# Kernel optimization log

Hardware: AMD Instinct MI355X
Metric: run time of the kernel (lower is better)

## Reference

```python
import jax, jax.numpy as jnp
import numpy as np

N, E, IN = 50000, 800000, 64
HC, FC1, FC2, FC3, OUT = 96, 256, 128, 64, 8
EPS = 1e-5


def setup_inputs() -> dict:
    key = jax.random.key(0)
    ks = jax.random.split(key, 24)
    def lin(k, fi, fo):
        # kaiming_uniform with relu gain: bound = sqrt(6/fi)
        b = np.sqrt(6.0 / fi)
        return jax.random.uniform(k, (fi, fo), jnp.float32, -b, b)
    inp = {
        'x': jax.random.normal(ks[0], (N, IN), jnp.float32),
        'edge_index': jax.random.randint(ks[1], (2, E), 0, N, jnp.int64),
        'w1': lin(ks[2], IN, HC), 'b1': jnp.zeros((HC,), jnp.float32),
        'g1': jax.random.uniform(ks[3], (HC,), jnp.float32, 0.5, 1.5), 'be1': jax.random.normal(ks[4], (HC,), jnp.float32) * 0.1,
        'w2': lin(ks[5], HC, HC), 'b2': jnp.zeros((HC,), jnp.float32),
        'g2': jax.random.uniform(ks[6], (HC,), jnp.float32, 0.5, 1.5), 'be2': jax.random.normal(ks[7], (HC,), jnp.float32) * 0.1,
        'w3': lin(ks[8], HC, HC), 'b3': jnp.zeros((HC,), jnp.float32),
        'g3': jax.random.uniform(ks[9], (HC,), jnp.float32, 0.5, 1.5), 'be3': jax.random.normal(ks[10], (HC,), jnp.float32) * 0.1,
        'lw1': lin(ks[11], HC, FC1), 'lb1': jnp.zeros((FC1,), jnp.float32),
        'lw2': lin(ks[12], FC1, FC2), 'lb2': jnp.zeros((FC2,), jnp.float32),
        'lw3': lin(ks[13], FC2, FC3), 'lb3': jnp.zeros((FC3,), jnp.float32),
        'lw4': lin(ks[14], FC3, OUT), 'lb4': jnp.zeros((OUT,), jnp.float32),
    }
    return inp


def _gcn(x, w, b, src, dst, norm):
    # GCNConv: out[dst] += norm_e * (x @ w)[src]; then + bias
    h = x @ w
    msg = h[src] * norm[:, None]
    return jax.ops.segment_sum(msg, dst, num_segments=N) + b


def _bn_eval(x, g, be):
    # eval-mode BatchNorm1d with running_mean=0, running_var=1
    return x / jnp.sqrt(1.0 + EPS) * g + be


def reference(x, edge_index, w1, b1, g1, be1, w2, b2, g2, be2, w3, b3, g3, be3,
              lw1, lb1, lw2, lb2, lw3, lb3, lw4, lb4):
    loops = jnp.arange(N, dtype=edge_index.dtype)
    src = jnp.concatenate([edge_index[0], loops])
    dst = jnp.concatenate([edge_index[1], loops])
    deg = jax.ops.segment_sum(jnp.ones_like(src, jnp.float32), dst, num_segments=N)
    dinv = jax.lax.rsqrt(deg)  # deg >= 1 due to self loops
    norm = dinv[src] * dinv[dst]

    h = jax.nn.relu(_bn_eval(_gcn(x, w1, b1, src, dst, norm), g1, be1))
    h = jax.nn.relu(_bn_eval(_gcn(h, w2, b2, src, dst, norm), g2, be2))
    h = jax.nn.relu(_bn_eval(_gcn(h, w3, b3, src, dst, norm), g3, be3))
    h = jax.nn.relu(h @ lw1 + lb1)
    h = jax.nn.relu(h @ lw2 + lb2)
    h = jax.nn.relu(h @ lw3 + lb3)
    return h @ lw4 + lb4
```

## Files before the change

kernel.cpp:

```cpp
#include <hip/hip_runtime.h>


#define GN 50000
#define GE 800000
#define NPART 98
#define PSLOT 9216
#define CHK 2048

typedef __attribute__((ext_vector_type(8))) short bf16x8;
typedef __attribute__((ext_vector_type(4))) float floatx4;
typedef __attribute__((ext_vector_type(2))) float floatx2;
typedef __attribute__((ext_vector_type(4))) unsigned int uintx4;

__device__ __forceinline__ float ar1_b2f(unsigned short h) {
    return __uint_as_float(((unsigned)h) << 16);
}
__device__ __forceinline__ unsigned short ar1_f2b(float f) {
    unsigned u = __float_as_uint(f);
    u = u + 0x7FFFu + ((u >> 16) & 1u);
    return (unsigned short)(u >> 16);
}
__device__ __forceinline__ floatx2 ar1_up2(unsigned w) {
    floatx2 t;
    t[0] = __uint_as_float(w << 16);
    t[1] = __uint_as_float(w & 0xFFFF0000u);
    return t;
}

__device__ __forceinline__ int ar1_det64(const int* ei) {
    int l = (int)threadIdx.x & 63;
    int nz = 0;
#pragma unroll
    for (int k = 0; k < 4; k++)
        nz += (ei[2 * (l + 64 * k) + 1] != 0) ? 1 : 0;
#pragma unroll
    for (int o = 1; o < 64; o <<= 1)
        nz += __shfl_xor(nz, o, 64);
    return (nz < 8) ? 1 : 0;
}
__device__ __forceinline__ int ar1_detf32(const unsigned short* xw) {
    int l = (int)threadIdx.x & 63;
    int c = 0;
#pragma unroll
    for (int k = 0; k < 4; k++) {
        unsigned short w = xw[2 * (l + 64 * k)];
        int ex = (w >> 7) & 0xFF;
        if (w == 0 || (ex >= 90 && ex <= 150)) c++;
    }
#pragma unroll
    for (int o = 1; o < 64; o <<= 1)
        c += __shfl_xor(c, o, 64);
    return (c > 200) ? 0 : 1;
}

struct PackAll {
    const void* src[7];
    unsigned short* dst[7];
    int K[7], M[7], start[8];
};
struct SmallCvt {
    const void* src[4];
    float* dst[4];
    int n[4];
    const void* gb[9];
    float* ss[6];
};

__global__ __launch_bounds__(256)
void Arthur1_16458314678864_kernel(PackAll pa, SmallCvt sc,
                                   const int* __restrict__ ei,
                                   const unsigned short* __restrict__ xw,
                                   int* flagI, int* flagF,
                                   int* __restrict__ gcur,
                                   unsigned int* __restrict__ pairs,
                                   unsigned short* __restrict__ xb,
                                   unsigned short* __restrict__ bufA,
                                   unsigned short* __restrict__ bufB,
                                   float* __restrict__ dinvp) {
    int b = (int)blockIdx.x;
    int tid = (int)threadIdx.x;
    if (b < 391) {
        __shared__ int cnt[NPART], base[NPART], cur[NPART];
        for (int i = tid; i < NPART; i += 256) { cnt[i] = 0; cur[i] = 0; }
        int is64 = ar1_det64(ei);
        __syncthreads();
        int e0 = b * CHK;
        unsigned pk[8]; int q[8];
#pragma unroll
        for (int k = 0; k < 8; k++) {
            int e = e0 + k * 256 + tid;
            q[k] = -1; pk[k] = 0;
            if (e < GE) {
                int s = is64 ? ei[2 * e] : ei[e];
                int d = is64 ? ei[2 * (GE + e)] : ei[GE + e];
                if ((unsigned)s < (unsigned)GN && (unsigned)d < (unsigned)GN) {
                    int qq = d >> 9;
                    q[k] = qq;
                    pk[k] = (unsigned)s | ((unsigned)(d & 511) << 17);
                    atomicAdd(&cnt[qq], 1);
                }
            }
        }
        __syncthreads();
        for (int i = tid; i < NPART; i += 256)
            base[i] = (cnt[i] > 0) ? atomicAdd(&gcur[i], cnt[i]) : 0;
        __syncthreads();
#pragma unroll
        for (int k = 0; k < 8; k++) {
            if (q[k] >= 0) {
                int r = base[q[k]] + atomicAdd(&cur[q[k]], 1);
                if (r < PSLOT) pairs[(size_t)q[k] * PSLOT + r] = pk[k];
            }
        }
    } else if (b < 436) {
        int f = ar1_detf32(xw);
        int frag_g = (b - 391) * 4 + (tid >> 6);
        if (frag_g >= 178) return;
        int w = 0;
        while (w < 6 && frag_g >= pa.start[w + 1]) w++;
        int frag = frag_g - pa.start[w];
        int K = pa.K[w], M = pa.M[w];
        int lane = tid & 63;
        int nch = K >> 5;
        int t = frag / nch, c = frag - t * nch;
        int n = t * 16 + (lane & 15);
        int k0 = c * 32 + (lane >> 4) * 8;
        unsigned short* o = pa.dst[w] + ((size_t)frag * 64 + lane) * 8;
        for (int j = 0; j < 8; j++) {
            unsigned short v = 0;
            if (n < M) {
                int idx = (k0 + j) * M + n;
                v = f ? ar1_f2b(((const float*)pa.src[w])[idx])
                      : ((const unsigned short*)pa.src[w])[idx];
            }
            o[j] = v;
        }
    } else if (b == 436) {
        int f = ar1_detf32(xw);
        int i64 = ar1_det64(ei);
        if (tid == 0) { flagI[0] = i64; flagF[0] = f; dinvp[GN] = 0.f; }
        if (tid < 96) {
            bufA[(size_t)GN * 96 + tid] = 0;
            bufB[(size_t)GN * 96 + tid] = 0;
        }
        if (tid >= 96 && tid < 160) xb[(size_t)GN * 64 + (tid - 96)] = 0;
        const float C = 0.9999950000374997f;
        for (int s = 0; s < 4; s++) {
            for (int i = tid; i < sc.n[s]; i += 256) {
                float v = f ? ((const float*)sc.src[s])[i]
                            : ar1_b2f(((const unsigned short*)sc.src[s])[i]);
                sc.dst[s][i] = v;
            }
        }
        for (int k = 0; k < 3; k++) {
            for (int i = tid; i < 96; i += 256) {
                float bb, g, be;
                if (f) {
                    bb = ((const float*)sc.gb[3 * k + 0])[i];
                    g  = ((const float*)sc.gb[3 * k + 1])[i];
                    be = ((const float*)sc.gb[3 * k + 2])[i];
                } else {
                    bb = ar1_b2f(((const unsigned short*)sc.gb[3 * k + 0])[i]);
                    g  = ar1_b2f(((const unsigned short*)sc.gb[3 * k + 1])[i]);
                    be = ar1_b2f(((const unsigned short*)sc.gb[3 * k + 2])[i]);
                }
                sc.ss[2 * k + 0][i] = C * g;
                sc.ss[2 * k + 1][i] = bb * C * g + be;
            }
        }
    } else {
        int f = ar1_detf32(xw);
        size_t t = (size_t)(b - 437) * 256 + (size_t)tid;
        size_t i0 = t * 8;
        if (i0 < (size_t)GN * 64) {
            bf16x8 o;
            if (f) {
                const float* xf = (const float*)xw;
                floatx4 a = *((const floatx4*)(xf + i0));
                floatx4 c = *((const floatx4*)(xf + i0 + 4));
#pragma unroll
                for (int j = 0; j < 4; j++) {
                    o[j]     = (short)ar1_f2b(a[j]);
                    o[4 + j] = (short)ar1_f2b(c[j]);
                }
            } else {
                o = *((const bf16x8*)(xw + i0));
            }
            *((bf16x8*)(xb + i0)) = o;
        }
    }
}

__global__ __launch_bounds__(256)
void ar1_csr(const unsigned int* __restrict__ pairs, const int* __restrict__ gcur,
             int* __restrict__ csr, int* __restrict__ indeg,
             int* __restrict__ offs, float* __restrict__ dinv,
             unsigned short* __restrict__ xb) {
    __shared__ int ncnt[512], pre[512], cur[512], psum[16], red[256];
    int p = (int)blockIdx.x, tid = (int)threadIdx.x;
    red[tid] = (tid < p && tid < NPART) ? gcur[tid] : 0;
    __syncthreads();
    for (int o = 128; o > 0; o >>= 1) {
        if (tid < o) red[tid] += red[tid + o];
        __syncthreads();
    }
    int gbase = red[0];
    int cntE = gcur[p];
    if (cntE > PSLOT) cntE = PSLOT;
    for (int i = tid; i < 512; i += 256) ncnt[i] = 0;
    __syncthreads();
    const unsigned int* pp = pairs + (size_t)p * PSLOT;
    for (int i = tid; i < cntE; i += 256) atomicAdd(&ncnt[pp[i] >> 17], 1);
    __syncthreads();
    if (tid < 16) {
        int s = 0;
        for (int j = tid * 32; j < tid * 32 + 32; j++) { pre[j] = s; s += ncnt[j]; }
        psum[tid] = s;
    }
    __syncthreads();
    if (tid == 0) {
        int s = 0;
        for (int j = 0; j < 16; j++) { int t = psum[j]; psum[j] = s; s += t; }
    }
    __syncthreads();
    if (tid < 16)
        for (int j = tid * 32; j < tid * 32 + 32; j++) pre[j] += psum[tid];
    __syncthreads();
    for (int j = tid; j < 512; j += 256) {
        cur[j] = pre[j];
        int node = p * 512 + j;
        if (node < GN) {
            indeg[node] = ncnt[j];
            offs[node] = gbase + pre[j];
            dinv[node] = rsqrtf((float)(ncnt[j] + 1));
        }
    }
    __syncthreads();
    for (int i = tid; i < cntE; i += 256) {
        unsigned v = pp[i];
        int r = atomicAdd(&cur[v >> 17], 1);
        csr[gbase + r] = (int)(v & 0x1FFFFu);
    }
    for (int i = tid; i < 512 * 8; i += 256) {
        int j = i >> 3, c = i & 7;
        int node = p * 512 + j;
        if (node < GN) {
            float sc = rsqrtf((float)(ncnt[j] + 1));
            bf16x8 v = *((bf16x8*)(xb + (size_t)node * 64 + c * 8));
#pragma unroll
            for (int jj = 0; jj < 8; jj++)
                v[jj] = (short)ar1_f2b(sc * ar1_b2f((unsigned short)v[jj]));
            *((bf16x8*)(xb + (size_t)node * 64 + c * 8)) = v;
        }
    }
}

__global__ __launch_bounds__(512, 8)
void ar1_ag64g(const unsigned short* __restrict__ Xb, const int* __restrict__ offs,
               const int* __restrict__ indeg, const int* __restrict__ csr,
               const float* __restrict__ dinv,
               const unsigned short* __restrict__ Bp,
               const float* __restrict__ scale, const float* __restrict__ shift,
               unsigned short* __restrict__ C) {
    __shared__ unsigned short AL[16 * 72];
    int tid = (int)threadIdx.x, wv = tid >> 6, lane = tid & 63;
    int nb = (int)blockIdx.x * 8;
    int node = nb + wv;
    int chunk = lane & 7, eslot = lane >> 3;
    float di = dinv[node];
    int off = offs[node], cnt = indeg[node];

    floatx2 acc2[4];
#pragma unroll
    for (int d = 0; d < 4; d++) acc2[d] = (floatx2){0.f, 0.f};

    for (int base = 0; base < cnt; base += 16) {
        int ss[2];
#pragma unroll
        for (int k = 0; k < 2; k++) {
            int e = base + k * 8 + eslot;
            ss[k] = (e < cnt) ? csr[off + e] : GN;
        }
        uintx4 hh[2];
#pragma unroll
        for (int k = 0; k < 2; k++)
            hh[k] = *((const uintx4*)(Xb + (size_t)ss[k] * 64 + chunk * 8));
#pragma unroll
        for (int k = 0; k < 2; k++)
#pragma unroll
            for (int d = 0; d < 4; d++)
                acc2[d] += ar1_up2(hh[k][d]);
    }
#pragma unroll
    for (int d = 0; d < 4; d++)
#pragma unroll
        for (int c = 0; c < 2; c++) {
            acc2[d][c] += __shfl_xor(acc2[d][c], 8, 64);
            acc2[d][c] += __shfl_xor(acc2[d][c], 16, 64);
            acc2[d][c] += __shfl_xor(acc2[d][c], 32, 64);
        }
    if (eslot == 0) {
        bf16x8 h = *((const bf16x8*)(Xb + (size_t)node * 64 + chunk * 8));
        bf16x8 o;
#pragma unroll
        for (int j = 0; j < 8; j++)
            o[j] = (short)ar1_f2b(di * (acc2[j >> 1][j & 1] +
                                        ar1_b2f((unsigned short)h[j])));
        *((bf16x8*)(AL + (size_t)wv * 72 + chunk * 8)) = o;
    }
    __syncthreads();

    if (wv < 6) {
        int m = lane & 15, quad = lane >> 4, t = wv;
        floatx4 g = (floatx4){0.f, 0.f, 0.f, 0.f};
#pragma unroll
        for (int c = 0; c < 2; c++) {
            bf16x8 a = *((const bf16x8*)(AL + (size_t)m * 72 + c * 32 + quad * 8));
            bf16x8 bfr = *((const bf16x8*)(Bp + ((size_t)(t * 2 + c) * 64 + lane) * 8));
            g = __builtin_amdgcn_mfma_f32_16x16x32_bf16(a, bfr, g, 0, 0, 0);
        }
        if (quad < 2) {
#pragma unroll
            for (int r = 0; r < 4; r++) {
                int row = nb + quad * 4 + r;
                int col = t * 16 + m;
                float v = g[r] * scale[col] + shift[col];
                C[(size_t)row * 96 + col] = ar1_f2b(dinv[row] * fmaxf(v, 0.f));
            }
        }
    }
}

__global__ __launch_bounds__(512, 8)
void ar1_ag96g(const unsigned short* __restrict__ H, const int* __restrict__ offs,
               const int* __restrict__ indeg, const int* __restrict__ csr,
               const float* __restrict__ dinv,
               const unsigned short* __restrict__ Bp,
               const float* __restrict__ scale, const float* __restrict__ shift,
               unsigned short* __restrict__ C) {
    __shared__ unsigned short AL[16 * 104];
    int tid = (int)threadIdx.x, wv = tid >> 6, lane = tid & 63;
    int nb = (int)blockIdx.x * 8;
    int node = nb + wv;
    int chunk = lane % 12, eslot = lane / 12;
    float di = dinv[node];
    int off = offs[node], cnt = indeg[node];

    floatx2 acc2[4];
#pragma unroll
    for (int d = 0; d < 4; d++) acc2[d] = (floatx2){0.f, 0.f};

    if (lane < 48) {
        for (int base = 0; base < cnt; base += 16) {
            int ss[4];
#pragma unroll
            for (int k = 0; k < 4; k++) {
                int e = base + k * 4 + eslot;
                ss[k] = (e < cnt) ? csr[off + e] : GN;
            }
            uintx4 hh[4];
#pragma unroll
            for (int k = 0; k < 4; k++)
                hh[k] = *((const uintx4*)(H + (size_t)ss[k] * 96 + chunk * 8));
#pragma unroll
            for (int k = 0; k < 4; k++)
#pragma unroll
                for (int d = 0; d < 4; d++)
                    acc2[d] += ar1_up2(hh[k][d]);
        }
    }
#pragma unroll
    for (int d = 0; d < 4; d++)
#pragma unroll
        for (int c = 0; c < 2; c++) {
            float a1 = __shfl(acc2[d][c], lane + 12, 64);
            float a2 = __shfl(acc2[d][c], lane + 24, 64);
            float a3 = __shfl(acc2[d][c], lane + 36, 64);
            acc2[d][c] += a1 + a2 + a3;
        }
    if (lane < 12) {
        bf16x8 hs = *((const bf16x8*)(H + (size_t)node * 96 + chunk * 8));
        bf16x8 o;
#pragma unroll
        for (int j = 0; j < 8; j++)
            o[j] = (short)ar1_f2b(di * (acc2[j >> 1][j & 1] +
                                        ar1_b2f((unsigned short)hs[j])));
        *((bf16x8*)(AL + (size_t)wv * 104 + chunk * 8)) = o;
    }
    __syncthreads();

    if (wv < 6) {
        int m = lane & 15, quad = lane >> 4, t = wv;
        floatx4 g = (floatx4){0.f, 0.f, 0.f, 0.f};
#pragma unroll
        for (int c = 0; c < 3; c++) {
            bf16x8 a = *((const bf16x8*)(AL + (size_t)m * 104 + c * 32 + quad * 8));
            bf16x8 bfr = *((const bf16x8*)(Bp + ((size_t)(t * 3 + c) * 64 + lane) * 8));
            g = __builtin_amdgcn_mfma_f32_16x16x32_bf16(a, bfr, g, 0, 0, 0);
        }
        if (quad < 2) {
#pragma unroll
            for (int r = 0; r < 4; r++) {
                int row = nb + quad * 4 + r;
                int col = t * 16 + m;
                float v = g[r] * scale[col] + shift[col];
                C[(size_t)row * 96 + col] = ar1_f2b(dinv[row] * fmaxf(v, 0.f));
            }
        }
    }
}

__global__ __launch_bounds__(512, 8)
void ar1_agmlp(const unsigned short* __restrict__ H, const int* __restrict__ offs,
               const int* __restrict__ indeg, const int* __restrict__ csr,
               const float* __restrict__ dinv,
               const unsigned short* __restrict__ b2w,
               const float* __restrict__ sc3, const float* __restrict__ sh3,
               const unsigned short* __restrict__ b3,
               const unsigned short* __restrict__ b4,
               const unsigned short* __restrict__ b5,
               const unsigned short* __restrict__ b6,
               const float* __restrict__ lb0, const float* __restrict__ lb1,
               const float* __restrict__ lb2, const float* __restrict__ lb3,
               void* __restrict__ out, const int* __restrict__ f32out) {
    __shared__ unsigned short AL[16 * 104];
    __shared__ unsigned short H0[16 * 104];
    __shared__ unsigned short H1[16 * 264];
    __shared__ unsigned short H2[16 * 136];
    __shared__ unsigned short H3[16 * 72];
    int tid = (int)threadIdx.x, wv = tid >> 6, lane = tid & 63;
    int nb = (int)blockIdx.x * 8;
    int node = nb + wv;
    int m = lane & 15, quad = lane >> 4;

    {
        int chunk = lane % 12, eslot = lane / 12;
        float di = dinv[node];
        int off = offs[node], cnt = indeg[node];
        floatx2 acc2[4];
#pragma unroll
        for (int d = 0; d < 4; d++) acc2[d] = (floatx2){0.f, 0.f};
        if (lane < 48) {
            for (int base = 0; base < cnt; base += 16) {
                int ss[4];
#pragma unroll
                for (int k = 0; k < 4; k++) {
                    int e = base + k * 4 + eslot;
                    ss[k] = (e < cnt) ? csr[off + e] : GN;
                }
                uintx4 hh[4];
#pragma unroll
                for (int k = 0; k < 4; k++)
                    hh[k] = *((const uintx4*)(H + (size_t)ss[k] * 96 + chunk * 8));
#pragma unroll
                for (int k = 0; k < 4; k++)
#pragma unroll
                    for (int d = 0; d < 4; d++)
                        acc2[d] += ar1_up2(hh[k][d]);
            }
        }
#pragma unroll
        for (int d = 0; d < 4; d++)
#pragma unroll
            for (int c = 0; c < 2; c++) {
                float a1 = __shfl(acc2[d][c], lane + 12, 64);
                float a2 = __shfl(acc2[d][c], lane + 24, 64);
                float a3 = __shfl(acc2[d][c], lane + 36, 64);
                acc2[d][c] += a1 + a2 + a3;
            }
        if (lane < 12) {
            bf16x8 hs = *((const bf16x8*)(H + (size_t)node * 96 + chunk * 8));
            bf16x8 o;
#pragma unroll
            for (int j = 0; j < 8; j++)
                o[j] = (short)ar1_f2b(di * (acc2[j >> 1][j & 1] +
                                            ar1_b2f((unsigned short)hs[j])));
            *((bf16x8*)(AL + (size_t)wv * 104 + chunk * 8)) = o;
        }
    }
    __syncthreads();

    if (wv < 6) {
        int t = wv;
        floatx4 g = (floatx4){0.f, 0.f, 0.f, 0.f};
#pragma unroll
        for (int c = 0; c < 3; c++) {
            bf16x8 a = *((const bf16x8*)(AL + (size_t)m * 104 + c * 32 + quad * 8));
            bf16x8 bfr = *((const bf16x8*)(b2w + ((size_t)(t * 3 + c) * 64 + lane) * 8));
            g = __builtin_amdgcn_mfma_f32_16x16x32_bf16(a, bfr, g, 0, 0, 0);
        }
#pragma unroll
        for (int r = 0; r < 4; r++) {
            int col = t * 16 + m;
            float v = g[r] * sc3[col] + sh3[col];
            H0[(quad * 4 + r) * 104 + col] = ar1_f2b(fmaxf(v, 0.f));
        }
    }
    __syncthreads();

    {
#pragma unroll
        for (int tt = 0; tt < 2; tt++) {
            int t = wv + tt * 8;
            floatx4 g = (floatx4){0.f, 0.f, 0.f, 0.f};
#pragma unroll
            for (int c = 0; c < 3; c++) {
                bf16x8 a = *((const bf16x8*)(H0 + (size_t)m * 104 + c * 32 + quad * 8));
                bf16x8 bfr = *((const bf16x8*)(b3 + ((size_t)(t * 3 + c) * 64 + lane) * 8));
                g = __builtin_amdgcn_mfma_f32_16x16x32_bf16(a, bfr, g, 0, 0, 0);
            }
#pragma unroll
            for (int r = 0; r < 4; r++) {
                int col = t * 16 + m;
                H1[(quad * 4 + r) * 264 + col] = ar1_f2b(fmaxf(g[r] + lb0[col], 0.f));
            }
        }
    }
    __syncthreads();

    {
        int t = wv;
        floatx4 g = (floatx4){0.f, 0.f, 0.f, 0.f};
#pragma unroll
        for (int c = 0; c < 8; c++) {
            bf16x8 a = *((const bf16x8*)(H1 + (size_t)m * 264 + c * 32 + quad * 8));
            bf16x8 bfr = *((const bf16x8*)(b4 + ((size_t)(t * 8 + c) * 64 + lane) * 8));
            g = __builtin_amdgcn_mfma_f32_16x16x32_bf16(a, bfr, g, 0, 0, 0);
        }
#pragma unroll
        for (int r = 0; r < 4; r++) {
            int col = t * 16 + m;
            H2[(quad * 4 + r) * 136 + col] = ar1_f2b(fmaxf(g[r] + lb1[col], 0.f));
        }
    }
    __syncthreads();

    if (wv < 4) {
        int t = wv;
        floatx4 g = (floatx4){0.f, 0.f, 0.f, 0.f};
#pragma unroll
        for (int c = 0; c < 4; c++) {
            bf16x8 a = *((const bf16x8*)(H2 + (size_t)m * 136 + c * 32 + quad * 8));
            bf16x8 bfr = *((const bf16x8*)(b5 + ((size_t)(t * 4 + c) * 64 + lane) * 8));
            g = __builtin_amdgcn_mfma_f32_16x16x32_bf16(a, bfr, g, 0, 0, 0);
        }
#pragma unroll
        for (int r = 0; r < 4; r++) {
            int col = t * 16 + m;
            H3[(quad * 4 + r) * 72 + col] = ar1_f2b(fmaxf(g[r] + lb2[col], 0.f));
        }
    }
    __syncthreads();

    if (wv == 0) {
        floatx4 g = (floatx4){0.f, 0.f, 0.f, 0.f};
#pragma unroll
        for (int c = 0; c < 2; c++) {
            bf16x8 a = *((const bf16x8*)(H3 + (size_t)m * 72 + c * 32 + quad * 8));
            bf16x8 bfr = *((const bf16x8*)(b6 + ((size_t)c * 64 + lane) * 8));
            g = __builtin_amdgcn_mfma_f32_16x16x32_bf16(a, bfr, g, 0, 0, 0);
        }
        int wf32 = f32out[0];
        if (quad < 2) {
#pragma unroll
            for (int r = 0; r < 4; r++) {
                int row = nb + quad * 4 + r;
                if (m < 8) {
                    float v = g[r] + lb3[m];
                    if (wf32) ((float*)out)[(size_t)row * 8 + m] = v;
                    else ((unsigned short*)out)[(size_t)row * 8 + m] = ar1_f2b(v);
                }
            }
        }
    }
}

extern "C" void kernel_launch(void* const* d_in, const int* in_sizes, int n_in,
                              void* d_out, int out_size, void* d_ws, size_t ws_size,
                              hipStream_t stream) {
    (void)in_sizes; (void)n_in; (void)out_size;

    char* p = (char*)d_ws;
    unsigned short* bufA = (unsigned short*)p; p += (size_t)(GN + 1) * 96 * 2;
    unsigned short* bufB = (unsigned short*)p; p += (size_t)(GN + 1) * 96 * 2;
    unsigned short* xb   = (unsigned short*)p; p += (size_t)(GN + 1) * 64 * 2;
    unsigned int* pairs = (unsigned int*)p; p += (size_t)NPART * PSLOT * 4;
    int* indeg  = (int*)p;    p += (size_t)GN * 4;
    int* offs   = (int*)p;    p += (size_t)GN * 4;
    float* dinv = (float*)p;  p += (size_t)GN * 4 + 64;
    int* csr    = (int*)p;    p += (size_t)GE * 4;
    int* gcur   = (int*)p;    p += 1024;
    int* flagI  = (int*)p;    p += 1024;
    int* flagF  = (int*)p;    p += 1024;
    unsigned short* bpArena = (unsigned short*)p; p += 91136 * 2;
    float* fArena = (float*)p; p += 2048 * 4;
    size_t need = (size_t)(p - (char*)d_ws);
    if (ws_size < need) {
        hipMemsetAsync(d_out, 0x41, (size_t)GN * 8 * 2, stream);
        return;
    }

    unsigned short* bp[7];
    int bpn[7] = {6144, 9216, 9216, 24576, 32768, 8192, 1024};
    {
        unsigned short* q = bpArena;
        for (int i = 0; i < 7; i++) { bp[i] = q; q += bpn[i]; }
    }

    float* lb[4]; float* ss[6];
    {
        float* q = fArena;
        int ln[4] = {256, 128, 64, 8};
        for (int i = 0; i < 4; i++) { lb[i] = q; q += ln[i]; }
        for (int i = 0; i < 6; i++) { ss[i] = q; q += 96; }
    }

    const int* ei = (const int*)d_in[1];
    const unsigned short* xw = (const unsigned short*)d_in[0];

    hipMemsetAsync(gcur, 0, NPART * 4, stream);
    {
        PackAll pa;
        int wsrc[7] = {2, 6, 10, 14, 16, 18, 20};
        int Ks[7] = {64, 96, 96, 96, 256, 128, 64};
        int Ms[7] = {96, 96, 96, 256, 128, 64, 8};
        int cum = 0;
        for (int i = 0; i < 7; i++) {
            pa.src[i] = d_in[wsrc[i]]; pa.dst[i] = bp[i];
            pa.K[i] = Ks[i]; pa.M[i] = Ms[i];
            pa.start[i] = cum;
            cum += (Ms[i] + 15) / 16 * (Ks[i] / 32);
        }
        pa.start[7] = cum;
        SmallCvt sc;
        int lsrc[4] = {15, 17, 19, 21};
        int ln[4] = {256, 128, 64, 8};
        for (int i = 0; i < 4; i++) { sc.src[i] = d_in[lsrc[i]]; sc.dst[i] = lb[i]; sc.n[i] = ln[i]; }
        int gsrc[9] = {3, 4, 5, 7, 8, 9, 11, 12, 13};
        for (int i = 0; i < 9; i++) sc.gb[i] = d_in[gsrc[i]];
        for (int i = 0; i < 6; i++) sc.ss[i] = ss[i];
        Arthur1_16458314678864_kernel<<<2000, 256, 0, stream>>>(
            pa, sc, ei, xw, flagI, flagF, gcur, pairs, xb, bufA, bufB, dinv);
    }
    ar1_csr<<<NPART, 256, 0, stream>>>(pairs, gcur, csr, indeg, offs, dinv, xb);

    const int FB = GN / 8;

    ar1_ag64g<<<FB, 512, 0, stream>>>(xb, offs, indeg, csr, dinv,
                                      bp[0], ss[0], ss[1], bufA);
    ar1_ag96g<<<FB, 512, 0, stream>>>(bufA, offs, indeg, csr, dinv,
                                      bp[1], ss[2], ss[3], bufB);
    ar1_agmlp<<<FB, 512, 0, stream>>>(bufB, offs, indeg, csr, dinv,
                                      bp[2], ss[4], ss[5],
                                      bp[3], bp[4], bp[5], bp[6],
                                      lb[0], lb[1], lb[2], lb[3], d_out, flagF);
}
```

Before: 287.5 us.

## Process two nodes per wave in fused GCN aggregate kernels to fill MFMA tiles

Each 512-thread block now aggregates 16 nodes instead of 8, with each wave gathering neighbours for two nodes at once. All 16 rows of the 16x16 MFMA tile now hold real data rather than half being padding, and the block count is halved. For the 96-wide kernels the per-node unroll drops from 4 to 2 edges per iteration, so the number of loads in flight per wave stays about the same while spread across two nodes. The cost is more registers for the doubled accumulators and a loop bound set by the larger of the two node degrees.

```diff
diff --git a/kernel.cpp b/kernel.cpp
--- a/kernel.cpp
+++ b/kernel.cpp
@@ -264,49 +264,64 @@
                unsigned short* __restrict__ C) {
     __shared__ unsigned short AL[16 * 72];
     int tid = (int)threadIdx.x, wv = tid >> 6, lane = tid & 63;
-    int nb = (int)blockIdx.x * 8;
-    int node = nb + wv;
+    int nb = (int)blockIdx.x * 16;
+    int nodeA = nb + wv, nodeB = nb + wv + 8;
     int chunk = lane & 7, eslot = lane >> 3;
-    float di = dinv[node];
-    int off = offs[node], cnt = indeg[node];
-
-    floatx2 acc2[4];
-#pragma unroll
-    for (int d = 0; d < 4; d++) acc2[d] = (floatx2){0.f, 0.f};
-
-    for (int base = 0; base < cnt; base += 16) {
-        int ss[2];
+    float diA = dinv[nodeA], diB = dinv[nodeB];
+    int offA = offs[nodeA], cntA = indeg[nodeA];
+    int offB = offs[nodeB], cntB = indeg[nodeB];
+    int cmax = cntA > cntB ? cntA : cntB;
+
+    floatx2 aA[4], aB[4];
+#pragma unroll
+    for (int d = 0; d < 4; d++) { aA[d] = (floatx2){0.f, 0.f}; aB[d] = (floatx2){0.f, 0.f}; }
+
+    for (int base = 0; base < cmax; base += 16) {
+        int sA[2], sB[2];
 #pragma unroll
         for (int k = 0; k < 2; k++) {
             int e = base + k * 8 + eslot;
-            ss[k] = (e < cnt) ? csr[off + e] : GN;
-        }
-        uintx4 hh[2];
+            sA[k] = (e < cntA) ? csr[offA + e] : GN;
+            sB[k] = (e < cntB) ? csr[offB + e] : GN;
+        }
+        uintx4 hA[2], hB[2];
+#pragma unroll
+        for (int k = 0; k < 2; k++) {
+            hA[k] = *((const uintx4*)(Xb + (size_t)sA[k] * 64 + chunk * 8));
+            hB[k] = *((const uintx4*)(Xb + (size_t)sB[k] * 64 + chunk * 8));
+        }
 #pragma unroll
         for (int k = 0; k < 2; k++)
-            hh[k] = *((const uintx4*)(Xb + (size_t)ss[k] * 64 + chunk * 8));
-#pragma unroll
-        for (int k = 0; k < 2; k++)
-#pragma unroll
-            for (int d = 0; d < 4; d++)
-                acc2[d] += ar1_up2(hh[k][d]);
+#pragma unroll
+            for (int d = 0; d < 4; d++) {
+                aA[d] += ar1_up2(hA[k][d]);
+                aB[d] += ar1_up2(hB[k][d]);
+            }
     }
 #pragma unroll
     for (int d = 0; d < 4; d++)
 #pragma unroll
         for (int c = 0; c < 2; c++) {
-            acc2[d][c] += __shfl_xor(acc2[d][c], 8, 64);
-            acc2[d][c] += __shfl_xor(acc2[d][c], 16, 64);
-            acc2[d][c] += __shfl_xor(acc2[d][c], 32, 64);
+            aA[d][c] += __shfl_xor(aA[d][c], 8, 64);
+            aA[d][c] += __shfl_xor(aA[d][c], 16, 64);
+            aA[d][c] += __shfl_xor(aA[d][c], 32, 64);
+            aB[d][c] += __shfl_xor(aB[d][c], 8, 64);
+            aB[d][c] += __shfl_xor(aB[d][c], 16, 64);
+            aB[d][c] += __shfl_xor(aB[d][c], 32, 64);
         }
     if (eslot == 0) {
-        bf16x8 h = *((const bf16x8*)(Xb + (size_t)node * 64 + chunk * 8));
-        bf16x8 o;
-#pragma unroll
-        for (int j = 0; j < 8; j++)
-            o[j] = (short)ar1_f2b(di * (acc2[j >> 1][j & 1] +
-                                        ar1_b2f((unsigned short)h[j])));
-        *((bf16x8*)(AL + (size_t)wv * 72 + chunk * 8)) = o;
+        bf16x8 hsA = *((const bf16x8*)(Xb + (size_t)nodeA * 64 + chunk * 8));
+        bf16x8 hsB = *((const bf16x8*)(Xb + (size_t)nodeB * 64 + chunk * 8));
+        bf16x8 oA, oB;
+#pragma unroll
+        for (int j = 0; j < 8; j++) {
+            oA[j] = (short)ar1_f2b(diA * (aA[j >> 1][j & 1] +
+                                          ar1_b2f((unsigned short)hsA[j])));
+            oB[j] = (short)ar1_f2b(diB * (aB[j >> 1][j & 1] +
+                                          ar1_b2f((unsigned short)hsB[j])));
+        }
+        *((bf16x8*)(AL + (size_t)wv * 72 + chunk * 8)) = oA;
+        *((bf16x8*)(AL + (size_t)(wv + 8) * 72 + chunk * 8)) = oB;
     }
     __syncthreads();
 
@@ -319,14 +334,12 @@
             bf16x8 bfr = *((const bf16x8*)(Bp + ((size_t)(t * 2 + c) * 64 + lane) * 8));
             g = __builtin_amdgcn_mfma_f32_16x16x32_bf16(a, bfr, g, 0, 0, 0);
         }
-        if (quad < 2) {
-#pragma unroll
-            for (int r = 0; r < 4; r++) {
-                int row = nb + quad * 4 + r;
-                int col = t * 16 + m;
-                float v = g[r] * scale[col] + shift[col];
-                C[(size_t)row * 96 + col] = ar1_f2b(dinv[row] * fmaxf(v, 0.f));
-            }
+#pragma unroll
+        for (int r = 0; r < 4; r++) {
+            int row = nb + quad * 4 + r;
+            int col = t * 16 + m;
+            float v = g[r] * scale[col] + shift[col];
+            C[(size_t)row * 96 + col] = ar1_f2b(dinv[row] * fmaxf(v, 0.f));
         }
     }
 }
@@ -340,52 +353,68 @@
                unsigned short* __restrict__ C) {
     __shared__ unsigned short AL[16 * 104];
     int tid = (int)threadIdx.x, wv = tid >> 6, lane = tid & 63;
-    int nb = (int)blockIdx.x * 8;
-    int node = nb + wv;
+    int nb = (int)blockIdx.x * 16;
+    int nodeA = nb + wv, nodeB = nb + wv + 8;
     int chunk = lane % 12, eslot = lane / 12;
-    float di = dinv[node];
-    int off = offs[node], cnt = indeg[node];
-
-    floatx2 acc2[4];
-#pragma unroll
-    for (int d = 0; d < 4; d++) acc2[d] = (floatx2){0.f, 0.f};
+    float diA = dinv[nodeA], diB = dinv[nodeB];
+    int offA = offs[nodeA], cntA = indeg[nodeA];
+    int offB = offs[nodeB], cntB = indeg[nodeB];
+    int cmax = cntA > cntB ? cntA : cntB;
+
+    floatx2 aA[4], aB[4];
+#pragma unroll
+    for (int d = 0; d < 4; d++) { aA[d] = (floatx2){0.f, 0.f}; aB[d] = (floatx2){0.f, 0.f}; }
 
     if (lane < 48) {
-        for (int base = 0; base < cnt; base += 16) {
-            int ss[4];
-#pragma unroll
-            for (int k = 0; k < 4; k++) {
+        for (int base = 0; base < cmax; base += 8) {
+            int sA[2], sB[2];
+#pragma unroll
+            for (int k = 0; k < 2; k++) {
                 int e = base + k * 4 + eslot;
-                ss[k] = (e < cnt) ? csr[off + e] : GN;
-            }
-            uintx4 hh[4];
-#pragma unroll
-            for (int k = 0; k < 4; k++)
-                hh[k] = *((const uintx4*)(H + (size_t)ss[k] * 96 + chunk * 8));
-#pragma unroll
-            for (int k = 0; k < 4; k++)
-#pragma unroll
-                for (int d = 0; d < 4; d++)
-                    acc2[d] += ar1_up2(hh[k][d]);
+                sA[k] = (e < cntA) ? csr[offA + e] : GN;
+                sB[k] = (e < cntB) ? csr[offB + e] : GN;
+            }
+            uintx4 hA[2], hB[2];
+#pragma unroll
+            for (int k = 0; k < 2; k++) {
+                hA[k] = *((const uintx4*)(H + (size_t)sA[k] * 96 + chunk * 8));
+                hB[k] = *((const uintx4*)(H + (size_t)sB[k] * 96 + chunk * 8));
+            }
+#pragma unroll
+            for (int k = 0; k < 2; k++)
+#pragma unroll
+                for (int d = 0; d < 4; d++) {
+                    aA[d] += ar1_up2(hA[k][d]);
+                    aB[d] += ar1_up2(hB[k][d]);
+                }
         }
     }
 #pragma unroll
     for (int d = 0; d < 4; d++)
 #pragma unroll
         for (int c = 0; c < 2; c++) {
-            float a1 = __shfl(acc2[d][c], lane + 12, 64);
-            float a2 = __shfl(acc2[d][c], lane + 24, 64);
-            float a3 = __shfl(acc2[d][c], lane + 36, 64);
-            acc2[d][c] += a1 + a2 + a3;
+            float x1 = __shfl(aA[d][c], lane + 12, 64);
+            float x2 = __shfl(aA[d][c], lane + 24, 64);
+            float x3 = __shfl(aA[d][c], lane + 36, 64);
+            aA[d][c] += x1 + x2 + x3;
+            float y1 = __shfl(aB[d][c], lane + 12, 64);
+            float y2 = __shfl(aB[d][c], lane + 24, 64);
+            float y3 = __shfl(aB[d][c], lane + 36, 64);
+            aB[d][c] += y1 + y2 + y3;
         }
     if (lane < 12) {
-        bf16x8 hs = *((const bf16x8*)(H + (size_t)node * 96 + chunk * 8));
-        bf16x8 o;
-#pragma unroll
-        for (int j = 0; j < 8; j++)
-            o[j] = (short)ar1_f2b(di * (acc2[j >> 1][j & 1] +
-                                        ar1_b2f((unsigned short)hs[j])));
-        *((bf16x8*)(AL + (size_t)wv * 104 + chunk * 8)) = o;
+        bf16x8 hsA = *((const bf16x8*)(H + (size_t)nodeA * 96 + chunk * 8));
+        bf16x8 hsB = *((const bf16x8*)(H + (size_t)nodeB * 96 + chunk * 8));
+        bf16x8 oA, oB;
+#pragma unroll
+        for (int j = 0; j < 8; j++) {
+            oA[j] = (short)ar1_f2b(diA * (aA[j >> 1][j & 1] +
+                                          ar1_b2f((unsigned short)hsA[j])));
+            oB[j] = (short)ar1_f2b(diB * (aB[j >> 1][j & 1] +
+                                          ar1_b2f((unsigned short)hsB[j])));
+        }
+        *((bf16x8*)(AL + (size_t)wv * 104 + chunk * 8)) = oA;
+        *((bf16x8*)(AL + (size_t)(wv + 8) * 104 + chunk * 8)) = oB;
     }
     __syncthreads();
 
@@ -398,14 +427,12 @@
             bf16x8 bfr = *((const bf16x8*)(Bp + ((size_t)(t * 3 + c) * 64 + lane) * 8));
             g = __builtin_amdgcn_mfma_f32_16x16x32_bf16(a, bfr, g, 0, 0, 0);
         }
-        if (quad < 2) {
-#pragma unroll
-            for (int r = 0; r < 4; r++) {
-                int row = nb + quad * 4 + r;
-                int col = t * 16 + m;
-                float v = g[r] * scale[col] + shift[col];
-                C[(size_t)row * 96 + col] = ar1_f2b(dinv[row] * fmaxf(v, 0.f));
-            }
+#pragma unroll
+        for (int r = 0; r < 4; r++) {
+            int row = nb + quad * 4 + r;
+            int col = t * 16 + m;
+            float v = g[r] * scale[col] + shift[col];
+            C[(size_t)row * 96 + col] = ar1_f2b(dinv[row] * fmaxf(v, 0.f));
         }
     }
 }
@@ -429,53 +456,69 @@
     __shared__ unsigned short H2[16 * 136];
     __shared__ unsigned short H3[16 * 72];
     int tid = (int)threadIdx.x, wv = tid >> 6, lane = tid & 63;
-    int nb = (int)blockIdx.x * 8;
-    int node = nb + wv;
+    int nb = (int)blockIdx.x * 16;
     int m = lane & 15, quad = lane >> 4;
 
     {
+        int nodeA = nb + wv, nodeB = nb + wv + 8;
         int chunk = lane % 12, eslot = lane / 12;
-        float di = dinv[node];
-        int off = offs[node], cnt = indeg[node];
-        floatx2 acc2[4];
-#pragma unroll
-        for (int d = 0; d < 4; d++) acc2[d] = (floatx2){0.f, 0.f};
+        float diA = dinv[nodeA], diB = dinv[nodeB];
+        int offA = offs[nodeA], cntA = indeg[nodeA];
+        int offB = offs[nodeB], cntB = indeg[nodeB];
+        int cmax = cntA > cntB ? cntA : cntB;
+        floatx2 aA[4], aB[4];
+#pragma unroll
+        for (int d = 0; d < 4; d++) { aA[d] = (floatx2){0.f, 0.f}; aB[d] = (floatx2){0.f, 0.f}; }
         if (lane < 48) {
-            for (int base = 0; base < cnt; base += 16) {
-                int ss[4];
-#pragma unroll
-                for (int k = 0; k < 4; k++) {
+            for (int base = 0; base < cmax; base += 8) {
+                int sA[2], sB[2];
+#pragma unroll
+                for (int k = 0; k < 2; k++) {
                     int e = base + k * 4 + eslot;
-                    ss[k] = (e < cnt) ? csr[off + e] : GN;
+                    sA[k] = (e < cntA) ? csr[offA + e] : GN;
+                    sB[k] = (e < cntB) ? csr[offB + e] : GN;
                 }
-                uintx4 hh[4];
-#pragma unroll
-                for (int k = 0; k < 4; k++)
-                    hh[k] = *((const uintx4*)(H + (size_t)ss[k] * 96 + chunk * 8));
-#pragma unroll
-                for (int k = 0; k < 4; k++)
-#pragma unroll
-                    for (int d = 0; d < 4; d++)
-                        acc2[d] += ar1_up2(hh[k][d]);
+                uintx4 hA[2], hB[2];
+#pragma unroll
+                for (int k = 0; k < 2; k++) {
+                    hA[k] = *((const uintx4*)(H + (size_t)sA[k] * 96 + chunk * 8));
+                    hB[k] = *((const uintx4*)(H + (size_t)sB[k] * 96 + chunk * 8));
+                }
+#pragma unroll
+                for (int k = 0; k < 2; k++)
+#pragma unroll
+                    for (int d = 0; d < 4; d++) {
+                        aA[d] += ar1_up2(hA[k][d]);
+                        aB[d] += ar1_up2(hB[k][d]);
+                    }
             }
         }
 #pragma unroll
         for (int d = 0; d < 4; d++)
 #pragma unroll
             for (int c = 0; c < 2; c++) {
-                float a1 = __shfl(acc2[d][c], lane + 12, 64);
-                float a2 = __shfl(acc2[d][c], lane + 24, 64);
-                float a3 = __shfl(acc2[d][c], lane + 36, 64);
-                acc2[d][c] += a1 + a2 + a3;
+                float x1 = __shfl(aA[d][c], lane + 12, 64);
+                float x2 = __shfl(aA[d][c], lane + 24, 64);
+                float x3 = __shfl(aA[d][c], lane + 36, 64);
+                aA[d][c] += x1 + x2 + x3;
+                float y1 = __shfl(aB[d][c], lane + 12, 64);
+                float y2 = __shfl(aB[d][c], lane + 24, 64);
+                float y3 = __shfl(aB[d][c], lane + 36, 64);
+                aB[d][c] += y1 + y2 + y3;
             }
         if (lane < 12) {
-            bf16x8 hs = *((const bf16x8*)(H + (size_t)node * 96 + chunk * 8));
-            bf16x8 o;
-#pragma unroll
-            for (int j = 0; j < 8; j++)
-                o[j] = (short)ar1_f2b(di * (acc2[j >> 1][j & 1] +
-                                            ar1_b2f((unsigned short)hs[j])));
-            *((bf16x8*)(AL + (size_t)wv * 104 + chunk * 8)) = o;
+            bf16x8 hsA = *((const bf16x8*)(H + (size_t)nodeA * 96 + chunk * 8));
+            bf16x8 hsB = *((const bf16x8*)(H + (size_t)nodeB * 96 + chunk * 8));
+            bf16x8 oA, oB;
+#pragma unroll
+            for (int j = 0; j < 8; j++) {
+                oA[j] = (short)ar1_f2b(diA * (aA[j >> 1][j & 1] +
+                                              ar1_b2f((unsigned short)hsA[j])));
+                oB[j] = (short)ar1_f2b(diB * (aB[j >> 1][j & 1] +
+                                              ar1_b2f((unsigned short)hsB[j])));
+            }
+            *((bf16x8*)(AL + (size_t)wv * 104 + chunk * 8)) = oA;
+            *((bf16x8*)(AL + (size_t)(wv + 8) * 104 + chunk * 8)) = oB;
         }
     }
     __syncthreads();
@@ -561,15 +604,13 @@
             g = __builtin_amdgcn_mfma_f32_16x16x32_bf16(a, bfr, g, 0, 0, 0);
         }
         int wf32 = f32out[0];
-        if (quad < 2) {
-#pragma unroll
-            for (int r = 0; r < 4; r++) {
-                int row = nb + quad * 4 + r;
-                if (m < 8) {
-                    float v = g[r] + lb3[m];
-                    if (wf32) ((float*)out)[(size_t)row * 8 + m] = v;
-                    else ((unsigned short*)out)[(size_t)row * 8 + m] = ar1_f2b(v);
-                }
+#pragma unroll
+        for (int r = 0; r < 4; r++) {
+            int row = nb + quad * 4 + r;
+            if (m < 8) {
+                float v = g[r] + lb3[m];
+                if (wf32) ((float*)out)[(size_t)row * 8 + m] = v;
+                else ((unsigned short*)out)[(size_t)row * 8 + m] = ar1_f2b(v);
             }
         }
     }
@@ -644,7 +685,7 @@
     }
     ar1_csr<<<NPART, 256, 0, stream>>>(pairs, gcur, csr, indeg, offs, dinv, xb);
 
-    const int FB = GN / 8;
+    const int FB = GN / 16;
 
     ar1_ag64g<<<FB, 512, 0, stream>>>(xb, offs, indeg, csr, dinv,
                                       bp[0], ss[0], ss[1], bufA);
```

Result: no change. 291.6 us (+1.4%).
